# Performance work log

Measured on AMD Instinct MI355X. Metric: run time of the kernel, lower is better.

Reference implementation:

```python
import jax, jax.numpy as jnp
import numpy as np

B, D, L, G, K, U, OUT = 131072, 256, 3, 4, 128, 64, 10


def setup_inputs() -> dict:
    key = jax.random.key(0)
    k1, k2, k3, k4 = jax.random.split(key, 4)
    x = jax.random.normal(k1, (B, D), dtype=jnp.float32)
    # per-level, per-group input node coords into the previous level's output
    idx = jax.random.randint(k2, (L, G, K), 0, D, dtype=jnp.int32)
    # per-group kernels [fan_in, units] and biases [units], stacked
    W = jax.random.normal(k3, (L, G, K, U), dtype=jnp.float32) * 0.1
    b = jnp.zeros((L, G, U), dtype=jnp.float32)
    W_out = jax.random.normal(k4, (D, OUT), dtype=jnp.float32) * 0.1
    b_out = jnp.zeros((OUT,), dtype=jnp.float32)
    return {"x": x, "idx": idx, "W": W, "b": b, "W_out": W_out, "b_out": b_out}


def reference(x, idx, W, b, W_out, b_out):
    # Each topological level: for every dependency-group g, gather K scalar
    # columns from the previous level (the per-node slice+concat in the
    # original), tiny matmul [B,K]@[K,U] + bias, tanh; level output is the
    # concat of group outputs -> [B, G*U]. Groups share shapes, so they are
    # batched over axis g with a single einsum per level.
    h = x
    n_levels = W.shape[0]
    for l in range(n_levels):  # small fixed loop over topology levels
        gathered = h[:, idx[l]]                                  # [B, G, K]
        z = jnp.einsum('bgk,gku->bgu', gathered, W[l]) + b[l]    # [B, G, U]
        h = jnp.tanh(z).reshape(z.shape[0], -1)                  # [B, G*U]
    # output level: single group fed by all previous nodes, linear out activation
    return h @ W_out + b_out                                      # [B, OUT]
```

## Files before the change

kernel.cpp:

```cpp
#include <hip/hip_runtime.h>

typedef unsigned short ushort_t;
typedef __attribute__((ext_vector_type(8))) short short8;
typedef __attribute__((ext_vector_type(4))) float floatx4;

#define DD 256
#define LL 3
#define GG 4
#define KK 128
#define UU 64
#define OUTN 10
#define HSTRIDE 264
#define MROWS 128

__device__ __forceinline__ ushort_t f2bf(float f) {
  unsigned u = __builtin_bit_cast(unsigned, f);
  u = (u + 0x7FFFu + ((u >> 16) & 1u)) >> 16;
  return (ushort_t)u;
}

__device__ __forceinline__ unsigned pack_bf2(float lo, float hi) {
  unsigned a = __builtin_bit_cast(unsigned, hi) + 0x8000u;
  unsigned b = __builtin_bit_cast(unsigned, lo) + 0x8000u;
  return __builtin_amdgcn_perm(a, b, 0x07060302u);
}

__device__ __forceinline__ float fast_tanh(float x) {
  float e = __builtin_amdgcn_exp2f(x * 2.885390081777927f);
  return __builtin_fmaf(-2.0f, __builtin_amdgcn_rcpf(e + 1.0f), 1.0f);
}

__global__ __launch_bounds__(256) void prep_kernel(
    const int* __restrict__ idx, const float* __restrict__ W,
    const float* __restrict__ Wout, ushort_t* __restrict__ AT,
    ushort_t* __restrict__ WoT) {
  int b = blockIdx.x;
  int t = threadIdx.x;
  if (b < LL * DD) {
    int l = b >> 8, n = b & 255, g = n >> 6, u = n & 63;
    __shared__ int sidx[KK];
    __shared__ float sw[KK];
    if (t < KK) {
      sidx[t] = idx[(l * GG + g) * KK + t];
      sw[t]   = W[((size_t)((l * GG + g) * KK + t)) * UU + u];
    }
    __syncthreads();
    float s = 0.f;
#pragma unroll 8
    for (int j = 0; j < KK; j++) s += (sidx[j] == t) ? sw[j] : 0.f;
    AT[(b << 8) | t] = f2bf(s);
  } else {
    int e2 = (b - LL * DD) * 256 + t;
    int n = e2 >> 8, k = e2 & 255;
    WoT[e2] = (n < OUTN) ? f2bf(Wout[k * OUTN + n]) : (ushort_t)0;
  }
}

__global__ __launch_bounds__(256, 2) void fused_kernel(
    const float* __restrict__ x, const float* __restrict__ bias,
    const float* __restrict__ bout, const ushort_t* __restrict__ AT,
    const ushort_t* __restrict__ WoT, float* __restrict__ out) {
  __shared__ ushort_t hbuf[MROWS * HSTRIDE];

  const int tid  = threadIdx.x;
  const int wave = tid >> 6;
  const int lane = tid & 63;
  const int quad = lane >> 4;
  const int l16  = lane & 15;
  const long row0 = (long)blockIdx.x * MROWS;

  const float4* xv = (const float4*)(x + row0 * DD);
#pragma unroll
  for (int i = 0; i < 32; i++) {
    int f  = tid + i * 256;
    int r  = f >> 6;
    int c4 = f & 63;
    float4 v = xv[r * 64 + c4];
    uint2 w;
    w.x = pack_bf2(v.x, v.y);
    w.y = pack_bf2(v.z, v.w);
    *(uint2*)&hbuf[r * HSTRIDE + c4 * 4] = w;
  }
  __syncthreads();

#pragma unroll 1
  for (int l = 0; l < 3; l++) {
    const ushort_t* Ab = AT + l * (DD * DD) + (wave * UU + l16) * DD + quad * 8;
    const ushort_t* hsrc = hbuf + l16 * HSTRIDE + quad * 8;

    floatx4 acc[8][4];
#pragma unroll
    for (int nt = 0; nt < 4; nt++) {
      float4 bv = *(const float4*)&bias[(l * GG + wave) * UU + nt * 16 + quad * 4];
      floatx4 ini = {bv.x, bv.y, bv.z, bv.w};
#pragma unroll
      for (int mt = 0; mt < 8; mt++) acc[mt][nt] = ini;
    }

    short8 wf[4], wfn[4];
#pragma unroll
    for (int nt = 0; nt < 4; nt++) wf[nt] = *(const short8*)&Ab[nt * 16 * DD];

#pragma unroll
    for (int ks = 0; ks < 8; ks++) {
      if (ks < 7) {
#pragma unroll
        for (int nt = 0; nt < 4; nt++)
          wfn[nt] = *(const short8*)&Ab[nt * 16 * DD + (ks + 1) * 32];
      }
      short8 bf[8];
#pragma unroll
      for (int mt = 0; mt < 8; mt++)
        bf[mt] = *(const short8*)&hsrc[mt * 16 * HSTRIDE + ks * 32];
#pragma unroll
      for (int mt = 0; mt < 8; mt++)
#pragma unroll
        for (int nt = 0; nt < 4; nt++)
          acc[mt][nt] = __builtin_amdgcn_mfma_f32_16x16x32_bf16(wf[nt], bf[mt], acc[mt][nt], 0, 0, 0);
#pragma unroll
      for (int nt = 0; nt < 4; nt++) wf[nt] = wfn[nt];
    }
    __syncthreads();

#pragma unroll
    for (int nt = 0; nt < 4; nt++) {
#pragma unroll
      for (int mt = 0; mt < 8; mt++) {
        uint2 w;
        w.x = pack_bf2(fast_tanh(acc[mt][nt][0]), fast_tanh(acc[mt][nt][1]));
        w.y = pack_bf2(fast_tanh(acc[mt][nt][2]), fast_tanh(acc[mt][nt][3]));
        *(uint2*)&hbuf[(mt * 16 + l16) * HSTRIDE + wave * UU + nt * 16 + quad * 4] = w;
      }
    }
    __syncthreads();
  }

  short8 wof[8];
#pragma unroll
  for (int ks = 0; ks < 8; ks++)
    wof[ks] = *(const short8*)&WoT[l16 * DD + ks * 32 + quad * 8];

  const floatx4 zero = {0.f, 0.f, 0.f, 0.f};
#pragma unroll
  for (int s = 0; s < 2; s++) {
    floatx4 accf = zero;
#pragma unroll
    for (int ks = 0; ks < 8; ks++) {
      short8 bfr = *(const short8*)&hbuf[(wave * 32 + s * 16 + l16) * HSTRIDE + ks * 32 + quad * 8];
      accf = __builtin_amdgcn_mfma_f32_16x16x32_bf16(wof[ks], bfr, accf, 0, 0, 0);
    }
    const long obase = (row0 + wave * 32 + s * 16 + l16) * OUTN;
    if (quad < 2) {
      float4 p = {accf[0] + bout[quad * 4 + 0], accf[1] + bout[quad * 4 + 1],
                  accf[2] + bout[quad * 4 + 2], accf[3] + bout[quad * 4 + 3]};
      *(float4*)&out[obase + quad * 4] = p;
    } else if (quad == 2) {
      float2 p = {accf[0] + bout[8], accf[1] + bout[9]};
      *(float2*)&out[obase + 8] = p;
    }
  }
}

extern "C" void kernel_launch(void* const* d_in, const int* in_sizes, int n_in,
                              void* d_out, int out_size, void* d_ws, size_t ws_size,
                              hipStream_t stream) {
  const float* x    = (const float*)d_in[0];
  const int*   idx  = (const int*)d_in[1];
  const float* W    = (const float*)d_in[2];
  const float* b    = (const float*)d_in[3];
  const float* Wout = (const float*)d_in[4];
  const float* bout = (const float*)d_in[5];
  float* out = (float*)d_out;

  ushort_t* AT  = (ushort_t*)d_ws;
  ushort_t* WoT = AT + LL * DD * DD;

  prep_kernel<<<LL * DD + 16, 256, 0, stream>>>(idx, W, Wout, AT, WoT);
  fused_kernel<<<131072 / MROWS, 256, 0, stream>>>(x, b, bout, AT, WoT, out);
}
```

Baseline: 271.1 us.

## Use 512-thread blocks with 8 waves each computing 32 output columns

Doubles the block to 8 waves, so each wave computes a 32-column slice of the 256-wide level output instead of 64 columns, halving the per-wave accumulator count. The LDS B-fragment loads are now software-pipelined one tile ahead rather than all loaded up front. The output stage is split so each wave handles 16 rows. Lower register pressure should allow more waves per CU to hide latency. In exchange, each B fragment read from LDS is reused across only two MFMAs instead of four, which raises LDS traffic per FLOP.

```diff
diff --git a/kernel.cpp b/kernel.cpp
--- a/kernel.cpp
+++ b/kernel.cpp
@@ -12,6 +12,7 @@
 #define OUTN 10
 #define HSTRIDE 264
 #define MROWS 128
+#define NT 2
 
 __device__ __forceinline__ ushort_t f2bf(float f) {
   unsigned u = __builtin_bit_cast(unsigned, f);
@@ -56,7 +57,7 @@
   }
 }
 
-__global__ __launch_bounds__(256, 2) void fused_kernel(
+__global__ __launch_bounds__(512, 4) void fused_kernel(
     const float* __restrict__ x, const float* __restrict__ bias,
     const float* __restrict__ bout, const ushort_t* __restrict__ AT,
     const ushort_t* __restrict__ WoT, float* __restrict__ out) {
@@ -71,8 +72,8 @@
 
   const float4* xv = (const float4*)(x + row0 * DD);
 #pragma unroll
-  for (int i = 0; i < 32; i++) {
-    int f  = tid + i * 256;
+  for (int i = 0; i < 16; i++) {
+    int f  = tid + i * 512;
     int r  = f >> 6;
     int c4 = f & 63;
     float4 v = xv[r * 64 + c4];
@@ -85,51 +86,51 @@
 
 #pragma unroll 1
   for (int l = 0; l < 3; l++) {
-    const ushort_t* Ab = AT + l * (DD * DD) + (wave * UU + l16) * DD + quad * 8;
+    const ushort_t* Ab = AT + l * (DD * DD) + (wave * 32 + l16) * DD + quad * 8;
     const ushort_t* hsrc = hbuf + l16 * HSTRIDE + quad * 8;
 
-    floatx4 acc[8][4];
+    floatx4 acc[8][NT];
 #pragma unroll
-    for (int nt = 0; nt < 4; nt++) {
-      float4 bv = *(const float4*)&bias[(l * GG + wave) * UU + nt * 16 + quad * 4];
+    for (int nt = 0; nt < NT; nt++) {
+      float4 bv = *(const float4*)&bias[l * DD + wave * 32 + nt * 16 + quad * 4];
       floatx4 ini = {bv.x, bv.y, bv.z, bv.w};
 #pragma unroll
       for (int mt = 0; mt < 8; mt++) acc[mt][nt] = ini;
     }
 
-    short8 wf[4], wfn[4];
+    short8 wf[NT], wfn[NT];
 #pragma unroll
-    for (int nt = 0; nt < 4; nt++) wf[nt] = *(const short8*)&Ab[nt * 16 * DD];
+    for (int nt = 0; nt < NT; nt++) wf[nt] = *(const short8*)&Ab[nt * 16 * DD];
 
 #pragma unroll
     for (int ks = 0; ks < 8; ks++) {
       if (ks < 7) {
 #pragma unroll
-        for (int nt = 0; nt < 4; nt++)
+        for (int nt = 0; nt < NT; nt++)
           wfn[nt] = *(const short8*)&Ab[nt * 16 * DD + (ks + 1) * 32];
       }
-      short8 bf[8];
+      short8 bfc = *(const short8*)&hsrc[0 * 16 * HSTRIDE + ks * 32];
 #pragma unroll
-      for (int mt = 0; mt < 8; mt++)
-        bf[mt] = *(const short8*)&hsrc[mt * 16 * HSTRIDE + ks * 32];
+      for (int mt = 0; mt < 8; mt++) {
+        short8 bfn;
+        if (mt < 7) bfn = *(const short8*)&hsrc[(mt + 1) * 16 * HSTRIDE + ks * 32];
+        acc[mt][0] = __builtin_amdgcn_mfma_f32_16x16x32_bf16(wf[0], bfc, acc[mt][0], 0, 0, 0);
+        acc[mt][1] = __builtin_amdgcn_mfma_f32_16x16x32_bf16(wf[1], bfc, acc[mt][1], 0, 0, 0);
+        bfc = bfn;
+      }
 #pragma unroll
-      for (int mt = 0; mt < 8; mt++)
-#pragma unroll
-        for (int nt = 0; nt < 4; nt++)
-          acc[mt][nt] = __builtin_amdgcn_mfma_f32_16x16x32_bf16(wf[nt], bf[mt], acc[mt][nt], 0, 0, 0);
-#pragma unroll
-      for (int nt = 0; nt < 4; nt++) wf[nt] = wfn[nt];
+      for (int nt = 0; nt < NT; nt++) wf[nt] = wfn[nt];
     }
     __syncthreads();
 
 #pragma unroll
-    for (int nt = 0; nt < 4; nt++) {
+    for (int nt = 0; nt < NT; nt++) {
 #pragma unroll
       for (int mt = 0; mt < 8; mt++) {
         uint2 w;
         w.x = pack_bf2(fast_tanh(acc[mt][nt][0]), fast_tanh(acc[mt][nt][1]));
         w.y = pack_bf2(fast_tanh(acc[mt][nt][2]), fast_tanh(acc[mt][nt][3]));
-        *(uint2*)&hbuf[(mt * 16 + l16) * HSTRIDE + wave * UU + nt * 16 + quad * 4] = w;
+        *(uint2*)&hbuf[(mt * 16 + l16) * HSTRIDE + wave * 32 + nt * 16 + quad * 4] = w;
       }
     }
     __syncthreads();
@@ -140,24 +141,20 @@
   for (int ks = 0; ks < 8; ks++)
     wof[ks] = *(const short8*)&WoT[l16 * DD + ks * 32 + quad * 8];
 
-  const floatx4 zero = {0.f, 0.f, 0.f, 0.f};
+  floatx4 accf = {0.f, 0.f, 0.f, 0.f};
 #pragma unroll
-  for (int s = 0; s < 2; s++) {
-    floatx4 accf = zero;
-#pragma unroll
-    for (int ks = 0; ks < 8; ks++) {
-      short8 bfr = *(const short8*)&hbuf[(wave * 32 + s * 16 + l16) * HSTRIDE + ks * 32 + quad * 8];
-      accf = __builtin_amdgcn_mfma_f32_16x16x32_bf16(wof[ks], bfr, accf, 0, 0, 0);
-    }
-    const long obase = (row0 + wave * 32 + s * 16 + l16) * OUTN;
-    if (quad < 2) {
-      float4 p = {accf[0] + bout[quad * 4 + 0], accf[1] + bout[quad * 4 + 1],
-                  accf[2] + bout[quad * 4 + 2], accf[3] + bout[quad * 4 + 3]};
-      *(float4*)&out[obase + quad * 4] = p;
-    } else if (quad == 2) {
-      float2 p = {accf[0] + bout[8], accf[1] + bout[9]};
-      *(float2*)&out[obase + 8] = p;
-    }
+  for (int ks = 0; ks < 8; ks++) {
+    short8 bfr = *(const short8*)&hbuf[(wave * 16 + l16) * HSTRIDE + ks * 32 + quad * 8];
+    accf = __builtin_amdgcn_mfma_f32_16x16x32_bf16(wof[ks], bfr, accf, 0, 0, 0);
+  }
+  const long obase = (row0 + wave * 16 + l16) * OUTN;
+  if (quad < 2) {
+    float4 p = {accf[0] + bout[quad * 4 + 0], accf[1] + bout[quad * 4 + 1],
+                accf[2] + bout[quad * 4 + 2], accf[3] + bout[quad * 4 + 3]};
+    *(float4*)&out[obase + quad * 4] = p;
+  } else if (quad == 2) {
+    float2 p = {accf[0] + bout[8], accf[1] + bout[9]};
+    *(float2*)&out[obase + 8] = p;
   }
 }
 
@@ -176,5 +173,5 @@
   ushort_t* WoT = AT + LL * DD * DD;
 
   prep_kernel<<<LL * DD + 16, 256, 0, stream>>>(idx, W, Wout, AT, WoT);
-  fused_kernel<<<131072 / MROWS, 256, 0, stream>>>(x, b, bout, AT, WoT, out);
+  fused_kernel<<<131072 / MROWS, 512, 0, stream>>>(x, b, bout, AT, WoT, out);
 }
```

Result: faster. 258.2 us (-4.8%).
